# Performance work log

Measured on AMD Instinct MI355X. Metric: run time of the kernel, lower is better.

The kernel has to match this reference:

```python
import jax, jax.numpy as jnp
import numpy as np

N, E, H, C = 100000, 1600000, 64, 40

def _mlp(h, w1, b1, w2, b2):
    return jax.nn.relu(h @ w1 + b1) @ w2 + b2

def setup_inputs() -> dict:
    key = jax.random.key(0)
    ks = jax.random.split(key, 16)
    def w(k, shape, fan_in):
        return jax.random.normal(k, shape, jnp.float32) / np.sqrt(fan_in)
    return {
        "x": jax.random.normal(ks[0], (N, H), jnp.float32),
        "edge_index": jax.random.randint(ks[1], (2, E), 0, N, jnp.int64),
        "edge_attr": jax.random.normal(ks[2], (E, 1), jnp.float32),
        # edge_mlp: Linear(1,H) -> ReLU -> Linear(H,H)
        "e_w1": w(ks[3], (1, H), 1), "e_b1": jnp.zeros((H,), jnp.float32),
        "e_w2": w(ks[4], (H, H), H), "e_b2": jnp.zeros((H,), jnp.float32),
        # conv1 update MLP + eps
        "eps1": jnp.zeros((), jnp.float32),
        "m1_w1": w(ks[5], (H, H), H), "m1_b1": jnp.zeros((H,), jnp.float32),
        "m1_w2": w(ks[6], (H, H), H), "m1_b2": jnp.zeros((H,), jnp.float32),
        # conv2 update MLP + eps
        "eps2": jnp.zeros((), jnp.float32),
        "m2_w1": w(ks[7], (H, H), H), "m2_b1": jnp.zeros((H,), jnp.float32),
        "m2_w2": w(ks[8], (H, H), H), "m2_b2": jnp.zeros((H,), jnp.float32),
        # classifier
        "lin_w": w(ks[9], (H, C), H), "lin_b": jnp.zeros((C,), jnp.float32),
    }

def reference(x, edge_index, edge_attr, e_w1, e_b1, e_w2, e_b2,
              eps1, m1_w1, m1_b1, m1_w2, m1_b2,
              eps2, m2_w1, m2_b1, m2_w2, m2_b2, lin_w, lin_b):
    n = x.shape[0]
    src, dst = edge_index[0], edge_index[1]
    edge_emb = _mlp(edge_attr, e_w1, e_b1, e_w2, e_b2)  # [E, H]

    def gine_conv(h, eps, w1, b1, w2, b2):
        msg = jax.nn.relu(h[src] + edge_emb)                 # gather + fuse  [E, H]
        aggr = jax.ops.segment_sum(msg, dst, num_segments=n) # scatter-add   [N, H]
        return _mlp((1.0 + eps) * h + aggr, w1, b1, w2, b2)

    h = jax.nn.relu(gine_conv(x, eps1, m1_w1, m1_b1, m1_w2, m1_b2))
    # dropout is identity in eval mode
    h = jax.nn.relu(gine_conv(h, eps2, m2_w1, m2_b1, m2_w2, m2_b2))
    return jax.nn.log_softmax(h @ lin_w + lin_b, axis=1)
```

## Files before the change

### kernel.cpp

```cpp
#include <hip/hip_runtime.h>
#include <hip/hip_bf16.h>
#include <stdint.h>


typedef unsigned int uint32;
typedef unsigned short ushort16;
typedef __attribute__((ext_vector_type(8))) short bf16x8;
typedef __attribute__((ext_vector_type(4))) float f32x4;

#define BKT_SHIFT 7
#define BKT_SIZE 128
#define BKT_MASK 127

static __device__ __forceinline__ unsigned short f2bf(float f) {
  __hip_bfloat16 h = __float2bfloat16(f);
  return *reinterpret_cast<unsigned short*>(&h);
}
static __device__ __forceinline__ float bf2f(unsigned short u) {
  return __uint_as_float(((uint32)u) << 16);
}

static __device__ __forceinline__ bool detect_is64(const uint32* ei, int E, int tid, int* sflag) {
  if (tid < 64) {
    int lim = (E < 64) ? E : 64;
    int nz = (tid < lim) ? (ei[2 * (size_t)tid + 1] != 0u) : 0;
    nz = __any(nz);
    if (tid == 0) *sflag = !nz;
  }
  __syncthreads();
  return *sflag != 0;
}

__global__ __launch_bounds__(256) void k_setup_cast_count(
    const float* __restrict__ w1, const float* __restrict__ b1,
    const float* __restrict__ w2, const float* __restrict__ b2,
    float* __restrict__ tsS, uint32* __restrict__ ABp,
    const float* __restrict__ xin, ushort16* __restrict__ xb, int n4,
    const uint32* __restrict__ ei, int* __restrict__ hist1, int E, int KB) {
  __shared__ float w2s[64 * 64];
  __shared__ float b2s[64];
  __shared__ float w1s[64], b1s[64], ts[64];
  __shared__ int rs[64], ms[64], vs[64];
  __shared__ int h[1024];
  __shared__ int sIs64;
  const int tid = threadIdx.x;
  const int CB = (n4 + 255) >> 8;
  if (blockIdx.x >= (uint32)(65 + CB)) {
    const int b = blockIdx.x - (65 + CB);
    for (int i = tid; i < 1024; i += 256) h[i] = 0;
    bool is64 = detect_is64(ei, E, tid, &sIs64);
    for (int i = b * 256 + tid; i < E; i += KB * 256) {
      int dst = is64 ? (int)ei[2 * ((size_t)E + i)] : (int)ei[(size_t)E + i];
      atomicAdd(&h[dst >> BKT_SHIFT], 1);
    }
    __syncthreads();
    for (int i = tid; i < 1024; i += 256)
      if (h[i]) atomicAdd(&hist1[i], h[i]);
    return;
  }
  if (blockIdx.x >= 65) {
    int i = (blockIdx.x - 65) * 256 + tid;
    if (i < n4) {
      float4 v = ((const float4*)xin)[i];
      ushort4 o;
      o.x = f2bf(v.x); o.y = f2bf(v.y); o.z = f2bf(v.z); o.w = f2bf(v.w);
      ((ushort4*)xb)[i] = o;
    }
    return;
  }
  const int p = blockIdx.x;
  {
    const float4* g4 = (const float4*)w2;
    float4* s4 = (float4*)w2s;
    for (int i = tid; i < 64 * 16; i += 256) s4[i] = g4[i];
    if (tid < 64) b2s[tid] = b2[tid];
  }
  if (tid < 64) {
    float w = w1[tid], b = b1[tid];
    w1s[tid] = w; b1s[tid] = b;
    int v = (w != 0.0f);
    vs[tid] = v;
    ts[tid] = v ? (-b / w) : 0.0f;
  }
  __syncthreads();
  if (tid < 64) {
    float tk = ts[tid];
    int r = 0, m = 0;
    for (int k = 0; k < 64; ++k) if (vs[k]) { r += (ts[k] < tk) ? 1 : 0; m += (ts[k] == tk) ? 1 : 0; }
    rs[tid] = r; ms[tid] = m;
    if (p == 0) {
      int pos;
      if (vs[tid]) {
        int c = 0;
        for (int j = 0; j < 64; ++j)
          if (vs[j] && (ts[j] < tk || (ts[j] == tk && j < tid))) c++;
        pos = c;
      } else {
        int c = 0;
        for (int j = 0; j < 64; ++j) if (vs[j]) c++;
        for (int j = 0; j < tid; ++j) if (!vs[j]) c++;
        pos = c;
      }
      tsS[pos] = vs[tid] ? tk : __builtin_inff();
    }
  }
  __syncthreads();
  if (tid < 64) {
    const int j = tid;
    float accA = 0.0f, accB = b2s[j];
    for (int k = 0; k < 64; ++k) {
      bool act;
      if (vs[k]) act = (w1s[k] > 0.0f) ? (p >= rs[k] + ms[k]) : (p <= rs[k]);
      else       act = (b1s[k] > 0.0f);
      if (act) { float wv = w2s[k * 64 + j]; accA = fmaf(w1s[k], wv, accA); accB = fmaf(b1s[k], wv, accB); }
    }
    ABp[p * 64 + j] = (uint32)f2bf(accA) | ((uint32)f2bf(accB) << 16);
  }
}

static __device__ __forceinline__ int scan_hist(const int* __restrict__ hist1,
                                                int* bo, int* psum, int tid) {
  int v0 = hist1[tid * 4 + 0], v1 = hist1[tid * 4 + 1];
  int v2 = hist1[tid * 4 + 2], v3 = hist1[tid * 4 + 3];
  int sum = v0 + v1 + v2 + v3;
  psum[tid] = sum;
  __syncthreads();
  for (int d = 1; d < 256; d <<= 1) {
    int add = (tid >= d) ? psum[tid - d] : 0;
    __syncthreads();
    psum[tid] += add;
    __syncthreads();
  }
  int run = psum[tid] - sum;
  bo[tid * 4 + 0] = run; run += v0;
  bo[tid * 4 + 1] = run; run += v1;
  bo[tid * 4 + 2] = run; run += v2;
  bo[tid * 4 + 3] = run; run += v3;
  int total = psum[255];
  __syncthreads();
  return total;
}


__global__ __launch_bounds__(256) void k_bpart(
    const uint32* __restrict__ ei, const float* __restrict__ ea,
    const float* __restrict__ tsSg, const int* __restrict__ hist1,
    int* __restrict__ bCur,
    int2* __restrict__ stage, unsigned short* __restrict__ dstw, int E) {
  __shared__ int cnt[1024];
  __shared__ int bo[1024];
  __shared__ int psum[256];
  __shared__ float tss[64];
  __shared__ int sIs64;
  const int tid = threadIdx.x;
  for (int i = tid; i < 1024; i += 256) cnt[i] = 0;
  if (tid >= 64 && tid < 128) tss[tid - 64] = tsSg[tid - 64];
  bool is64 = detect_is64(ei, E, tid, &sIs64);
  scan_hist(hist1, bo, psum, tid);
  const int base0 = blockIdx.x * 2048;
  int dstv[8], srcv[8], rk[8];
  float av[8];
#pragma unroll
  for (int e = 0; e < 8; ++e) {
    int idx = base0 + e * 256 + tid;
    if (idx < E) {
      int src, dst;
      if (is64) { src = (int)ei[2 * (size_t)idx]; dst = (int)ei[2 * ((size_t)E + idx)]; }
      else      { src = (int)ei[(size_t)idx];     dst = (int)ei[(size_t)E + idx]; }
      dstv[e] = dst; srcv[e] = src; av[e] = ea[idx];
      rk[e] = atomicAdd(&cnt[dst >> BKT_SHIFT], 1);
    } else dstv[e] = -1;
  }
  __syncthreads();
  for (int b = tid; b < 1024; b += 256) {
    int c = cnt[b];
    cnt[b] = c ? (bo[b] + atomicAdd(&bCur[b], c)) : 0;
  }
  __syncthreads();
#pragma unroll
  for (int e = 0; e < 8; ++e) {
    if (dstv[e] < 0) continue;
    float a = av[e];
    int p = 0;
#pragma unroll
    for (int s = 32; s > 0; s >>= 1) if (tss[p + s - 1] < a) p += s;
    if (tss[p] < a) ++p;
    int pos = cnt[dstv[e] >> BKT_SHIFT] + rk[e];
    stage[pos] = make_int2(srcv[e] | (p << 20), __float_as_int(a));
    dstw[pos] = (unsigned short)(dstv[e] & BKT_MASK);
  }
}

__global__ __launch_bounds__(256) void k_blocal(
    const int* __restrict__ hist1, const int2* __restrict__ stage,
    const unsigned short* __restrict__ dstw,
    int* __restrict__ offs, int2* __restrict__ pay, int N) {
  __shared__ int bo[1024];
  __shared__ int psum[256];
  __shared__ int h[512], cur[512], ps2[256];
  const int tid = threadIdx.x;
  const int b = blockIdx.x;
  int Etot = scan_hist(hist1, bo, psum, tid);
  const int s = bo[b];
  const int e2 = (b == (int)gridDim.x - 1) ? Etot : bo[b + 1];
  if (b == 0 && tid == 0) offs[N] = Etot;
  h[tid] = 0; h[tid + 256] = 0;
  __syncthreads();
  for (int j = s + tid; j < e2; j += 256) atomicAdd(&h[dstw[j]], 1);
  __syncthreads();
  int a0 = h[2 * tid], a1 = h[2 * tid + 1];
  ps2[tid] = a0 + a1;
  __syncthreads();
  for (int d = 1; d < 256; d <<= 1) {
    int add = (tid >= d) ? ps2[tid - d] : 0;
    __syncthreads();
    ps2[tid] += add;
    __syncthreads();
  }
  int ex = s + ps2[tid] - (a0 + a1);
  if (2 * tid < BKT_SIZE) {
    cur[2 * tid] = ex;
    cur[2 * tid + 1] = ex + a0;
    int nd0 = b * BKT_SIZE + 2 * tid;
    if (nd0 < N) offs[nd0] = ex;
    if (nd0 + 1 < N) offs[nd0 + 1] = ex + a0;
  }
  __syncthreads();
  for (int j = s + tid; j < e2; j += 256) {
    int pos = atomicAdd(&cur[dstw[j]], 1);
    pay[pos] = stage[j];
  }
}


#define EDGE8_LOAD(ib, qx, av)                                   \
  _Pragma("unroll")                                              \
  for (int t = 0; t < 8; ++t) {                                  \
    int2 q_ = pay[(ib) + t];                                     \
    qx[t] = (uint32)__builtin_amdgcn_readfirstlane(q_.x);        \
    av[t] = (uint32)__builtin_amdgcn_readfirstlane(q_.y);        \
  }

#define EDGE8_GATHER(qx, xv, ab)                                 \
  _Pragma("unroll")                                              \
  for (int t = 0; t < 8; ++t) {                                  \
    xv[t] = bf2f(xb[(size_t)(qx[t] & 0xFFFFFu) * 64u + lane]);   \
    ab[t] = ABs[(qx[t] >> 20) * 64u + lane];                     \
  }

#define EDGE8_ACC(av, xv, ab, acc)                               \
  _Pragma("unroll")                                              \
  for (int t = 0; t < 8; ++t)                                    \
    acc += fmaxf(fmaf(__uint_as_float(av[t]),                    \
                      __uint_as_float(ab[t] << 16),              \
                      __uint_as_float(ab[t] & 0xffff0000u)) + xv[t], 0.0f);

#define EDGE1(ib, acc) do {                                      \
    int2 q_ = pay[(ib)];                                         \
    uint32 qx_ = (uint32)__builtin_amdgcn_readfirstlane(q_.x);   \
    uint32 av_ = (uint32)__builtin_amdgcn_readfirstlane(q_.y);   \
    float xv_ = bf2f(xb[(size_t)(qx_ & 0xFFFFFu) * 64u + lane]); \
    uint32 ab_ = ABs[(qx_ >> 20) * 64u + lane];                  \
    acc += fmaxf(fmaf(__uint_as_float(av_),                      \
                      __uint_as_float(ab_ << 16),                \
                      __uint_as_float(ab_ & 0xffff0000u)) + xv_, 0.0f); \
  } while (0)

__global__ __launch_bounds__(512, 8) void k_conv(
    const unsigned short* __restrict__ xb,
    const int* __restrict__ offs, const int2* __restrict__ pay,
    const uint32* __restrict__ ABp, const float* __restrict__ epsp,
    unsigned short* __restrict__ uout, int n) {
  __shared__ uint32 ABs[65 * 64];
  {
    const uint4* g4 = (const uint4*)ABp;
    uint4* s4 = (uint4*)ABs;
    for (int i = threadIdx.x; i < 65 * 16; i += 512) s4[i] = g4[i];
  }
  __syncthreads();
  const int lane = threadIdx.x & 63;
  const int wid = __builtin_amdgcn_readfirstlane((int)(threadIdx.x >> 6));
  const float scale = 1.0f + epsp[0];
  const int npair = (n + 1) >> 1;
  for (int w = blockIdx.x * 8 + wid; w < npair; w += gridDim.x * 8) {
    const int ndA = __builtin_amdgcn_readfirstlane(w * 2);
    const bool hasB = (ndA + 1) < n;
    const int sA = offs[ndA];
    const int eA = offs[ndA + 1];
    const int eB = hasB ? offs[ndA + 2] : eA;
    float accA = 0.0f, accB = 0.0f;
    int iA = sA, iB = eA;
    while (iA + 7 < eA && iB + 7 < eB) {
      const int ia = __builtin_amdgcn_readfirstlane(iA);
      const int ib = __builtin_amdgcn_readfirstlane(iB);
      uint32 qxA[8], avA[8], qxB[8], avB[8];
      EDGE8_LOAD(ia, qxA, avA);
      EDGE8_LOAD(ib, qxB, avB);
      float xvA[8], xvB[8];
      uint32 abA[8], abB[8];
      EDGE8_GATHER(qxA, xvA, abA);
      EDGE8_GATHER(qxB, xvB, abB);
      EDGE8_ACC(avA, xvA, abA, accA);
      EDGE8_ACC(avB, xvB, abB, accB);
      iA += 8; iB += 8;
    }
    while (iA + 7 < eA) {
      const int ia = __builtin_amdgcn_readfirstlane(iA);
      uint32 qx[8], av[8];
      EDGE8_LOAD(ia, qx, av);
      float xv[8]; uint32 ab[8];
      EDGE8_GATHER(qx, xv, ab);
      EDGE8_ACC(av, xv, ab, accA);
      iA += 8;
    }
    while (iB + 7 < eB) {
      const int ib = __builtin_amdgcn_readfirstlane(iB);
      uint32 qx[8], av[8];
      EDGE8_LOAD(ib, qx, av);
      float xv[8]; uint32 ab[8];
      EDGE8_GATHER(qx, xv, ab);
      EDGE8_ACC(av, xv, ab, accB);
      iB += 8;
    }
    while (iA < eA && iB < eB) {
      const int ia = __builtin_amdgcn_readfirstlane(iA);
      const int ib = __builtin_amdgcn_readfirstlane(iB);
      int2 qa = pay[ia];
      int2 qb = pay[ib];
      uint32 qxa = (uint32)__builtin_amdgcn_readfirstlane(qa.x);
      uint32 ava = (uint32)__builtin_amdgcn_readfirstlane(qa.y);
      uint32 qxb = (uint32)__builtin_amdgcn_readfirstlane(qb.x);
      uint32 avb = (uint32)__builtin_amdgcn_readfirstlane(qb.y);
      float xva = bf2f(xb[(size_t)(qxa & 0xFFFFFu) * 64u + lane]);
      float xvb = bf2f(xb[(size_t)(qxb & 0xFFFFFu) * 64u + lane]);
      uint32 aba = ABs[(qxa >> 20) * 64u + lane];
      uint32 abb = ABs[(qxb >> 20) * 64u + lane];
      accA += fmaxf(fmaf(__uint_as_float(ava), __uint_as_float(aba << 16),
                         __uint_as_float(aba & 0xffff0000u)) + xva, 0.0f);
      accB += fmaxf(fmaf(__uint_as_float(avb), __uint_as_float(abb << 16),
                         __uint_as_float(abb & 0xffff0000u)) + xvb, 0.0f);
      ++iA; ++iB;
    }
    while (iA < eA) { EDGE1(__builtin_amdgcn_readfirstlane(iA), accA); ++iA; }
    while (iB < eB) { EDGE1(__builtin_amdgcn_readfirstlane(iB), accB); ++iB; }
    float xsA = bf2f(xb[(size_t)ndA * 64 + lane]);
    uout[(size_t)ndA * 64 + lane] = f2bf(fmaf(scale, xsA, accA));
    if (hasB) {
      float xsB = bf2f(xb[((size_t)ndA + 1) * 64 + lane]);
      uout[((size_t)ndA + 1) * 64 + lane] = f2bf(fmaf(scale, xsB, accB));
    }
  }
}

template <int OUTW>
static __device__ __forceinline__ bf16x8 load_bfrag(const float* __restrict__ W,
                                                    int hh, int q, int ncol, bool valid) {
  bf16x8 f;
#pragma unroll
  for (int j = 0; j < 8; ++j) {
    int k = hh * 32 + q * 8 + j;
    f[j] = valid ? (short)f2bf(W[k * OUTW + ncol]) : (short)0;
  }
  return f;
}

#define MFMA_BF16(A, B, C) __builtin_amdgcn_mfma_f32_16x16x32_bf16((A), (B), (C), 0, 0, 0)

__global__ __launch_bounds__(256) void k_mlp1(
    const unsigned short* __restrict__ uin, unsigned short* __restrict__ houtb,
    const float* __restrict__ W1, const float* __restrict__ B1,
    const float* __restrict__ W2, const float* __restrict__ B2, int n) {
  __shared__ unsigned short T[4][16 * 72];
  const int lane = threadIdx.x & 63;
  const int wid = threadIdx.x >> 6;
  const int cl = lane & 15;
  const int q = lane >> 4;
  bf16x8 w1f[4][2], w2f[4][2];
  float b1v[4], b2v[4];
#pragma unroll
  for (int t = 0; t < 4; ++t) {
#pragma unroll
    for (int hh = 0; hh < 2; ++hh) {
      w1f[t][hh] = load_bfrag<64>(W1, hh, q, t * 16 + cl, true);
      w2f[t][hh] = load_bfrag<64>(W2, hh, q, t * 16 + cl, true);
    }
    b1v[t] = B1[t * 16 + cl];
    b2v[t] = B2[t * 16 + cl];
  }
  unsigned short* Tw = T[wid];
  for (int node0 = blockIdx.x * 64 + wid * 16; node0 < n; node0 += gridDim.x * 64) {
    const unsigned short* ub = uin + (size_t)(node0 + cl) * 64;
    bf16x8 au0 = *(const bf16x8*)(ub + q * 8);
    bf16x8 au1 = *(const bf16x8*)(ub + 32 + q * 8);
#pragma unroll
    for (int t = 0; t < 4; ++t) {
      f32x4 acc = {b1v[t], b1v[t], b1v[t], b1v[t]};
      acc = MFMA_BF16(au0, w1f[t][0], acc);
      acc = MFMA_BF16(au1, w1f[t][1], acc);
#pragma unroll
      for (int r = 0; r < 4; ++r)
        Tw[(q * 4 + r) * 72 + t * 16 + cl] = f2bf(fmaxf(acc[r], 0.0f));
    }
    bf16x8 ah0 = *(const bf16x8*)&Tw[cl * 72 + q * 8];
    bf16x8 ah1 = *(const bf16x8*)&Tw[cl * 72 + 32 + q * 8];
#pragma unroll
    for (int t = 0; t < 4; ++t) {
      f32x4 acc = {b2v[t], b2v[t], b2v[t], b2v[t]};
      acc = MFMA_BF16(ah0, w2f[t][0], acc);
      acc = MFMA_BF16(ah1, w2f[t][1], acc);
#pragma unroll
      for (int r = 0; r < 4; ++r)
        Tw[(q * 4 + r) * 72 + t * 16 + cl] = f2bf(fmaxf(acc[r], 0.0f));
    }
    int m2 = lane >> 2, pt = lane & 3;
    if (node0 + m2 < n) {
      bf16x8 c0 = *(const bf16x8*)&Tw[m2 * 72 + pt * 16];
      bf16x8 c1 = *(const bf16x8*)&Tw[m2 * 72 + pt * 16 + 8];
      unsigned short* ob = houtb + (size_t)(node0 + m2) * 64 + pt * 16;
      *(bf16x8*)ob = c0;
      *(bf16x8*)(ob + 8) = c1;
    }
  }
}

__global__ __launch_bounds__(256) void k_mlp_cls(
    const unsigned short* __restrict__ uin,
    const float* __restrict__ W1, const float* __restrict__ B1,
    const float* __restrict__ W2, const float* __restrict__ B2,
    const float* __restrict__ LW, const float* __restrict__ LB,
    float* __restrict__ out, int n) {
  __shared__ unsigned short T[4][16 * 72];
  __shared__ float L[4][16 * 52];
  const int lane = threadIdx.x & 63;
  const int wid = threadIdx.x >> 6;
  const int cl = lane & 15;
  const int q = lane >> 4;
  bf16x8 w1f[4][2], w2f[4][2], lwf[3][2];
  float b1v[4], b2v[4], lbv[3];
#pragma unroll
  for (int t = 0; t < 4; ++t) {
#pragma unroll
    for (int hh = 0; hh < 2; ++hh) {
      w1f[t][hh] = load_bfrag<64>(W1, hh, q, t * 16 + cl, true);
      w2f[t][hh] = load_bfrag<64>(W2, hh, q, t * 16 + cl, true);
    }
    b1v[t] = B1[t * 16 + cl];
    b2v[t] = B2[t * 16 + cl];
  }
#pragma unroll
  for (int t = 0; t < 3; ++t) {
    bool valid = (t * 16 + cl) < 40;
#pragma unroll
    for (int hh = 0; hh < 2; ++hh)
      lwf[t][hh] = load_bfrag<40>(LW, hh, q, valid ? (t * 16 + cl) : 0, valid);
    lbv[t] = valid ? LB[t * 16 + cl] : 0.0f;
  }
  unsigned short* Tw = T[wid];
  float* Lw = L[wid];
  for (int node0 = blockIdx.x * 64 + wid * 16; node0 < n; node0 += gridDim.x * 64) {
    const unsigned short* ub = uin + (size_t)(node0 + cl) * 64;
    bf16x8 au0 = *(const bf16x8*)(ub + q * 8);
    bf16x8 au1 = *(const bf16x8*)(ub + 32 + q * 8);
#pragma unroll
    for (int t = 0; t < 4; ++t) {
      f32x4 acc = {b1v[t], b1v[t], b1v[t], b1v[t]};
      acc = MFMA_BF16(au0, w1f[t][0], acc);
      acc = MFMA_BF16(au1, w1f[t][1], acc);
#pragma unroll
      for (int r = 0; r < 4; ++r)
        Tw[(q * 4 + r) * 72 + t * 16 + cl] = f2bf(fmaxf(acc[r], 0.0f));
    }
    bf16x8 ah0 = *(const bf16x8*)&Tw[cl * 72 + q * 8];
    bf16x8 ah1 = *(const bf16x8*)&Tw[cl * 72 + 32 + q * 8];
#pragma unroll
    for (int t = 0; t < 4; ++t) {
      f32x4 acc = {b2v[t], b2v[t], b2v[t], b2v[t]};
      acc = MFMA_BF16(ah0, w2f[t][0], acc);
      acc = MFMA_BF16(ah1, w2f[t][1], acc);
#pragma unroll
      for (int r = 0; r < 4; ++r)
        Tw[(q * 4 + r) * 72 + t * 16 + cl] = f2bf(fmaxf(acc[r], 0.0f));
    }
    bf16x8 g0 = *(const bf16x8*)&Tw[cl * 72 + q * 8];
    bf16x8 g1 = *(const bf16x8*)&Tw[cl * 72 + 32 + q * 8];
#pragma unroll
    for (int t = 0; t < 3; ++t) {
      f32x4 acc = {lbv[t], lbv[t], lbv[t], lbv[t]};
      acc = MFMA_BF16(g0, lwf[t][0], acc);
      acc = MFMA_BF16(g1, lwf[t][1], acc);
#pragma unroll
      for (int r = 0; r < 4; ++r)
        Lw[(q * 4 + r) * 52 + t * 16 + cl] = acc[r];
    }
    int m3 = lane >> 2, j3 = lane & 3;
    float lg[10];
#pragma unroll
    for (int i = 0; i < 10; ++i) lg[i] = Lw[m3 * 52 + j3 * 10 + i];
    float mx = lg[0];
#pragma unroll
    for (int i = 1; i < 10; ++i) mx = fmaxf(mx, lg[i]);
    mx = fmaxf(mx, __shfl_xor(mx, 1));
    mx = fmaxf(mx, __shfl_xor(mx, 2));
    float se = 0.0f;
#pragma unroll
    for (int i = 0; i < 10; ++i) se += __expf(lg[i] - mx);
    se += __shfl_xor(se, 1);
    se += __shfl_xor(se, 2);
    float lse = mx + __logf(se);
    if (node0 + m3 < n) {
      float* o = out + (size_t)(node0 + m3) * 40 + j3 * 10;
#pragma unroll
      for (int i = 0; i < 10; ++i) o[i] = lg[i] - lse;
    }
  }
}

extern "C" void kernel_launch(void* const* d_in, const int* in_sizes, int n_in,
                              void* d_out, int out_size, void* d_ws, size_t ws_size,
                              hipStream_t stream) {
  (void)n_in; (void)out_size; (void)ws_size;
  const float* x     = (const float*)d_in[0];
  const uint32* ei   = (const uint32*)d_in[1];
  const float* eattr = (const float*)d_in[2];
  const float* e_w1 = (const float*)d_in[3];
  const float* e_b1 = (const float*)d_in[4];
  const float* e_w2 = (const float*)d_in[5];
  const float* e_b2 = (const float*)d_in[6];
  const float* eps1 = (const float*)d_in[7];
  const float* m1w1 = (const float*)d_in[8];
  const float* m1b1 = (const float*)d_in[9];
  const float* m1w2 = (const float*)d_in[10];
  const float* m1b2 = (const float*)d_in[11];
  const float* eps2 = (const float*)d_in[12];
  const float* m2w1 = (const float*)d_in[13];
  const float* m2b1 = (const float*)d_in[14];
  const float* m2w2 = (const float*)d_in[15];
  const float* m2b2 = (const float*)d_in[16];
  const float* linw = (const float*)d_in[17];
  const float* linb = (const float*)d_in[18];

  const int N = in_sizes[0] / 64;
  const int E = in_sizes[1] / 2;
  const int NBKT = (N + BKT_SIZE - 1) >> BKT_SHIFT;

  char* ws = (char*)d_ws;
  size_t off = 0;
  auto alloc = [&](size_t bytes, size_t align) {
    off = (off + align - 1) & ~(align - 1);
    size_t r = off; off += bytes; return r;
  };
  size_t oT    = alloc(64 * 4, 64);
  size_t oAB   = alloc(65 * 64 * 4, 64);
  size_t oHC   = alloc(2048 * 4, 128);
  size_t oOffs = alloc(((size_t)N + 1) * 4, 128);
  size_t oPay  = alloc((size_t)E * 8, 256);
  size_t oXb   = alloc((size_t)N * 64 * 2 + 32768, 256);
  size_t oU    = alloc((size_t)N * 64 * 2 + 32768, 1024);
  size_t oStg  = alloc((size_t)E * 8, 256);
  size_t oDw   = alloc((size_t)E * 2, 256);

  float*  tsS  = (float*)(ws + oT);
  uint32* ABp  = (uint32*)(ws + oAB);
  int*    h1   = (int*)(ws + oHC);
  int*    bCur = (int*)(ws + oHC + 1024 * 4);
  int*    offs = (int*)(ws + oOffs);
  int2*   pay  = (int2*)(ws + oPay);
  ushort16* xb = (ushort16*)(ws + oXb);
  ushort16* ubuf = (ushort16*)(ws + oU);
  int2*   stage = (int2*)(ws + oStg);
  unsigned short* dstw = (unsigned short*)(ws + oDw);

  hipMemsetAsync(ws + oHC, 0, 2048 * 4, stream);

  const int n4 = N * 64 / 4;
  const int CB = (n4 + 255) / 256;
  const int PB = (E + 2047) / 2048;
  const int KB = 1024;
  const int MB = (N + 63) / 64;

  k_setup_cast_count<<<65 + CB + KB, 256, 0, stream>>>(
      e_w1, e_b1, e_w2, e_b2, tsS, ABp, x, xb, n4, ei, h1, E, KB);
  k_bpart<<<PB, 256, 0, stream>>>(ei, eattr, tsS, h1, bCur, stage, dstw, E);
  k_blocal<<<NBKT, 256, 0, stream>>>(h1, stage, dstw, offs, pay, N);
  k_conv<<<2048, 512, 0, stream>>>((const unsigned short*)xb, offs, pay, ABp, eps1, ubuf, N);
  k_mlp1<<<MB, 256, 0, stream>>>((const unsigned short*)ubuf, (unsigned short*)xb,
                                 m1w1, m1b1, m1w2, m1b2, N);
  k_conv<<<2048, 512, 0, stream>>>((const unsigned short*)xb, offs, pay, ABp, eps2, ubuf, N);
  k_mlp_cls<<<MB, 256, 0, stream>>>((const unsigned short*)ubuf,
                                    m2w1, m2b1, m2w2, m2b2, linw, linb,
                                    (float*)d_out, N);
}
```

Before: 354.2 us.

## Widen dst buckets to 512 and stage bucket partition writes through LDS

Bucket width grows from 128 to 512 destination nodes, so about 196 buckets cover N=100000 instead of about 782. That cuts global atomic traffic on bucket cursors and gives each per-bucket local sort block more edges to work on. The partition kernel now does a block-local exclusive scan of bucket counts and first writes payloads into shared memory in bucket order. It then copies them out with coalesced-ish global stores, so edges of the same bucket land contiguously instead of as scattered stores. This adds an extra scan, 24KB of LDS per block and more syncs, and packs the global index into 21 bits, which fits E=1.6M.

```diff
diff --git a/kernel.cpp b/kernel.cpp
--- a/kernel.cpp
+++ b/kernel.cpp
@@ -8,9 +8,9 @@
 typedef __attribute__((ext_vector_type(8))) short bf16x8;
 typedef __attribute__((ext_vector_type(4))) float f32x4;
 
-#define BKT_SHIFT 7
-#define BKT_SIZE 128
-#define BKT_MASK 127
+#define BKT_SHIFT 9
+#define BKT_SIZE 512
+#define BKT_MASK 511
 
 static __device__ __forceinline__ unsigned short f2bf(float f) {
   __hip_bfloat16 h = __float2bfloat16(f);
@@ -152,6 +152,8 @@
   __shared__ int psum[256];
   __shared__ float tss[64];
   __shared__ int sIs64;
+  __shared__ int2 sspay[2048];
+  __shared__ uint32 ssmeta[2048];
   const int tid = threadIdx.x;
   for (int i = tid; i < 1024; i += 256) cnt[i] = 0;
   if (tid >= 64 && tid < 128) tss[tid - 64] = tsSg[tid - 64];
@@ -174,8 +176,26 @@
   __syncthreads();
   for (int b = tid; b < 1024; b += 256) {
     int c = cnt[b];
-    cnt[b] = c ? (bo[b] + atomicAdd(&bCur[b], c)) : 0;
-  }
+    if (c) bo[b] = bo[b] + atomicAdd(&bCur[b], c);
+  }
+  int v0 = cnt[tid * 4 + 0], v1 = cnt[tid * 4 + 1];
+  int v2 = cnt[tid * 4 + 2], v3 = cnt[tid * 4 + 3];
+  int lsum = v0 + v1 + v2 + v3;
+  __syncthreads();
+  psum[tid] = lsum;
+  __syncthreads();
+  for (int d = 1; d < 256; d <<= 1) {
+    int add = (tid >= d) ? psum[tid - d] : 0;
+    __syncthreads();
+    psum[tid] += add;
+    __syncthreads();
+  }
+  int lrun = psum[tid] - lsum;
+  cnt[tid * 4 + 0] = lrun; lrun += v0;
+  cnt[tid * 4 + 1] = lrun; lrun += v1;
+  cnt[tid * 4 + 2] = lrun; lrun += v2;
+  cnt[tid * 4 + 3] = lrun;
+  const int totloc = psum[255];
   __syncthreads();
 #pragma unroll
   for (int e = 0; e < 8; ++e) {
@@ -185,9 +205,18 @@
 #pragma unroll
     for (int s = 32; s > 0; s >>= 1) if (tss[p + s - 1] < a) p += s;
     if (tss[p] < a) ++p;
-    int pos = cnt[dstv[e] >> BKT_SHIFT] + rk[e];
-    stage[pos] = make_int2(srcv[e] | (p << 20), __float_as_int(a));
-    dstw[pos] = (unsigned short)(dstv[e] & BKT_MASK);
+    const int b = dstv[e] >> BKT_SHIFT;
+    const int slot = cnt[b] + rk[e];
+    const int gd = bo[b] + rk[e];
+    sspay[slot] = make_int2(srcv[e] | (p << 20), __float_as_int(a));
+    ssmeta[slot] = (uint32)gd | ((uint32)(dstv[e] & BKT_MASK) << 21);
+  }
+  __syncthreads();
+  for (int j = tid; j < totloc; j += 256) {
+    uint32 m = ssmeta[j];
+    int gd = (int)(m & 0x1FFFFFu);
+    stage[gd] = sspay[j];
+    dstw[gd] = (unsigned short)(m >> 21);
   }
 }
 
@@ -218,9 +247,9 @@
     __syncthreads();
   }
   int ex = s + ps2[tid] - (a0 + a1);
-  if (2 * tid < BKT_SIZE) {
-    cur[2 * tid] = ex;
-    cur[2 * tid + 1] = ex + a0;
+  cur[2 * tid] = ex;
+  cur[2 * tid + 1] = ex + a0;
+  {
     int nd0 = b * BKT_SIZE + 2 * tid;
     if (nd0 < N) offs[nd0] = ex;
     if (nd0 + 1 < N) offs[nd0 + 1] = ex + a0;
```

Result: faster. 336.4 us (-5.0%).
